# Kernel tuning notes

Hardware: AMD Instinct MI355X
Metric: run time of the kernel (lower is better)

## Reference

```python
import jax, jax.numpy as jnp
import numpy as np

N = 50000
E = 800000
IN_C, HID_C, OUT_C = 512, 256, 64
K = 10
ALPHA = 0.1


def setup_inputs() -> dict:
    key = jax.random.key(0)
    k1, k2, k3, k4, k5, k6 = jax.random.split(key, 6)
    x = jax.random.normal(k1, (N, IN_C), dtype=jnp.float32)
    edge_index = jax.random.randint(k2, (2, E), 0, N, dtype=jnp.int64)
    # Linear params (torch nn.Linear: y = x @ W.T + b), kaiming-ish scale
    W1 = jax.random.normal(k3, (HID_C, IN_C), dtype=jnp.float32) / np.sqrt(IN_C)
    b1 = jax.random.normal(k4, (HID_C,), dtype=jnp.float32) * 0.01
    W2 = jax.random.normal(k5, (OUT_C, HID_C), dtype=jnp.float32) / np.sqrt(HID_C)
    b2 = jax.random.normal(k6, (OUT_C,), dtype=jnp.float32) * 0.01
    return {"x": x, "edge_index": edge_index, "W1": W1, "b1": b1, "W2": W2, "b2": b2}


def reference(x, edge_index, W1, b1, W2, b2):
    # MLP head (dropout is identity in eval mode)
    h = jax.nn.relu(x @ W1.T + b1)          # [N, HID_C]
    z = h @ W2.T + b2                        # [N, OUT_C]

    src = edge_index[0]                      # message source
    dst = edge_index[1]                      # message target (aggregation index)

    # GCN symmetric normalization with self-loops (PyG APPNP default)
    ones = jnp.ones((E,), dtype=z.dtype)
    deg = jax.ops.segment_sum(ones, dst, num_segments=N) + 1.0  # +1 for self-loop
    dinv = jax.lax.rsqrt(deg)                # deg^{-1/2}
    edge_norm = (dinv[src] * dinv[dst])[:, None]   # [E, 1]
    self_norm = (dinv * dinv)[:, None]             # [N, 1] self-loop weight

    def step(hcur, _):
        agg = jax.ops.segment_sum(hcur[src] * edge_norm, dst, num_segments=N)
        agg = agg + hcur * self_norm
        hnew = (1.0 - ALPHA) * agg + ALPHA * z
        return hnew, None

    h_final, _ = jax.lax.scan(step, z, None, length=K)
    return h_final
```

## Files before the change

kernel.cpp:

```cpp
#include <hip/hip_runtime.h>

typedef __bf16 bf16x8 __attribute__((ext_vector_type(8)));
typedef float f32x4 __attribute__((ext_vector_type(4)));
typedef short short8 __attribute__((ext_vector_type(8)));

__device__ __forceinline__ unsigned short f2bf_u(float f) {
    unsigned u = __builtin_bit_cast(unsigned, f);
    u += 0x7FFFu + ((u >> 16) & 1u);
    return (unsigned short)(u >> 16);
}
__device__ __forceinline__ float bf2f(unsigned short h) {
    unsigned u = ((unsigned)h) << 16;
    return __builtin_bit_cast(float, u);
}
__device__ __forceinline__ float i2f(int b) { return __builtin_bit_cast(float, b); }

#define GLOAD_LDS16(gsrc, ldst)                                                        \
    __builtin_amdgcn_global_load_lds((const __attribute__((address_space(1))) void*)(gsrc), \
                                     (__attribute__((address_space(3))) void*)(ldst), 16, 0, 0)

__global__ __launch_bounds__(256)
void prep_a(const void* __restrict__ ei, const float* __restrict__ W1,
            const float* __restrict__ W2, int* __restrict__ flag,
            short* __restrict__ W1h, short* __restrict__ W1l,
            short* __restrict__ W2h, short* __restrict__ W2l) {
    const int tid = threadIdx.x;
    const int gtid = blockIdx.x * 256 + tid;
    const int gsize = gridDim.x * 256;
    if (blockIdx.x == 0) {
        unsigned v = 0;
        for (int i = tid * 2 + 1; i < 2048; i += 512) v |= ((const unsigned*)ei)[i];
        if (v) atomicOr(flag, 1);
    }
    const int n1 = 256 * 512, n2 = 64 * 256;
    for (int i = gtid; i < n1; i += gsize) {
        float w0 = W1[i];
        unsigned short h = f2bf_u(w0);
        W1h[i] = (short)h;
        W1l[i] = (short)f2bf_u(w0 - bf2f(h));
    }
    for (int i = gtid; i < n2; i += gsize) {
        float w0 = W2[i];
        unsigned short h = f2bf_u(w0);
        W2h[i] = (short)h;
        W2l[i] = (short)f2bf_u(w0 - bf2f(h));
    }
}

__global__ void convert_count_kernel(const void* __restrict__ edges, const int* __restrict__ flag,
                                     int* __restrict__ src, int* __restrict__ dst,
                                     int* __restrict__ counts, int E) {
    int e = blockIdx.x * 256 + threadIdx.x;
    if (e >= E) return;
    int s, d;
    if (*flag) { const int* p = (const int*)edges; s = p[e]; d = p[E + e]; }
    else       { const long long* p = (const long long*)edges; s = (int)p[e]; d = (int)p[E + e]; }
    src[e] = s;
    dst[e] = d;
    atomicAdd(&counts[d], 1);
}

__global__ void bsum_dinv_kernel(const int* __restrict__ counts, float* __restrict__ dinv,
                                 int* __restrict__ bs, int n) {
    __shared__ int sdata[256];
    int i = blockIdx.x * 256 + threadIdx.x;
    int v = (i < n) ? counts[i] : 0;
    if (i < n) dinv[i] = rsqrtf((float)v + 1.0f);
    sdata[threadIdx.x] = v;
    __syncthreads();
    #pragma unroll
    for (int off = 128; off > 0; off >>= 1) {
        if (threadIdx.x < off) sdata[threadIdx.x] += sdata[threadIdx.x + off];
        __syncthreads();
    }
    if (threadIdx.x == 0) bs[blockIdx.x] = sdata[0];
}

__global__ void scanbs_kernel(const int* __restrict__ bs, int* __restrict__ bsoff, int nb) {
    __shared__ int sdata[256];
    int tid = threadIdx.x;
    int v = (tid < nb) ? bs[tid] : 0;
    sdata[tid] = v;
    __syncthreads();
    #pragma unroll
    for (int off = 1; off < 256; off <<= 1) {
        int t = (tid >= off) ? sdata[tid - off] : 0;
        __syncthreads();
        sdata[tid] += t;
        __syncthreads();
    }
    if (tid < nb) bsoff[tid] = sdata[tid] - v;
}

__global__ void scanblock_kernel(const int* __restrict__ counts, const int* __restrict__ bsoff,
                                 int* __restrict__ rowptr, int* __restrict__ cursor, int n) {
    __shared__ int sdata[256];
    int tid = threadIdx.x;
    int i = blockIdx.x * 256 + tid;
    int v = (i < n) ? counts[i] : 0;
    sdata[tid] = v;
    __syncthreads();
    #pragma unroll
    for (int off = 1; off < 256; off <<= 1) {
        int t = (tid >= off) ? sdata[tid - off] : 0;
        __syncthreads();
        sdata[tid] += t;
        __syncthreads();
    }
    int excl = bsoff[blockIdx.x] + sdata[tid] - v;
    if (i < n) { rowptr[i] = excl; cursor[i] = excl; }
    if (i == n - 1) rowptr[n] = excl + v;
}

__global__ void fill_kernel(const int* __restrict__ src, const int* __restrict__ dst,
                            const float* __restrict__ dinv, int* __restrict__ cursor,
                            int2* __restrict__ csr, int E) {
    int e = blockIdx.x * 256 + threadIdx.x;
    if (e >= E) return;
    int s = src[e], d = dst[e];
    int pos = atomicAdd(&cursor[d], 1);
    float w = dinv[s] * dinv[d];
    csr[pos] = make_int2(s, __builtin_bit_cast(int, w));
}

__global__ __launch_bounds__(512)
void gemm1f_k(const float* __restrict__ x, const short* __restrict__ Bh,
              const short* __restrict__ Bl, const float* __restrict__ bias,
              short* __restrict__ C, int M) {
    extern __shared__ short lds[];
    short* sA  = lds;
    short* sBh = lds + 16384;
    short* sBl = lds + 49152;
    const int KDIM = 512, LDC = 256;
    const int tid = threadIdx.x, lane = tid & 63, wave = tid >> 6;
    const int wr = wave >> 2, wc = wave & 3;
    const int m0 = blockIdx.x * 128;
    const int lr = lane & 15, lk = lane >> 4;
    const int l8r = lane >> 3, l8u = lane & 7;
    const int tr = tid >> 3, tk = tid & 7;

    f32x4 acc[4][4];
    #pragma unroll
    for (int mi = 0; mi < 4; ++mi)
        #pragma unroll
        for (int ni = 0; ni < 4; ++ni) acc[mi][ni] = {0.f, 0.f, 0.f, 0.f};

    float4 fa[2][2];

    auto a_load = [&](int k0) {
        #pragma unroll
        for (int p = 0; p < 2; ++p) {
            int row = p * 64 + tr;
            int grow = m0 + row; if (grow > M - 1) grow = M - 1;
            const float* s = x + (size_t)grow * KDIM + k0 + tk * 8;
            fa[p][0] = *reinterpret_cast<const float4*>(s);
            fa[p][1] = *reinterpret_cast<const float4*>(s + 4);
        }
    };
    auto a_write = [&](int buf) {
        #pragma unroll
        for (int p = 0; p < 2; ++p) {
            int row = p * 64 + tr;
            short8 sh;
            sh[0] = (short)f2bf_u(fa[p][0].x); sh[1] = (short)f2bf_u(fa[p][0].y);
            sh[2] = (short)f2bf_u(fa[p][0].z); sh[3] = (short)f2bf_u(fa[p][0].w);
            sh[4] = (short)f2bf_u(fa[p][1].x); sh[5] = (short)f2bf_u(fa[p][1].y);
            sh[6] = (short)f2bf_u(fa[p][1].z); sh[7] = (short)f2bf_u(fa[p][1].w);
            *reinterpret_cast<short8*>(&sA[buf * 8192 + row * 64 + ((tk ^ (row & 7)) << 3)]) = sh;
        }
    };
    auto b_dma = [&](int buf, int k0) {
        #pragma unroll
        for (int p = 0; p < 4; ++p) {
            int row = p * 64 + wave * 8 + l8r;
            size_t goff = (size_t)row * KDIM + k0 + ((l8u ^ (row & 7)) << 3);
            GLOAD_LDS16(Bh + goff, sBh + buf * 16384 + (p * 64 + wave * 8) * 64);
            GLOAD_LDS16(Bl + goff, sBl + buf * 16384 + (p * 64 + wave * 8) * 64);
        }
    };

    a_load(0);
    b_dma(0, 0);
    asm volatile("s_waitcnt vmcnt(0)" ::: "memory");
    a_write(0);
    __syncthreads();

    int cur = 0;
    #pragma unroll 1
    for (int t = 0; t < 8; ++t) {
        const bool pf = (t < 7);
        if (pf) {
            a_load((t + 1) * 64);
            b_dma(cur ^ 1, (t + 1) * 64);
        }
        #pragma unroll
        for (int ks = 0; ks < 2; ++ks) {
            int kg = ks * 4 + lk;
            bf16x8 af[4], bhf[4], blf[4];
            #pragma unroll
            for (int mi = 0; mi < 4; ++mi) {
                int row = wr * 64 + mi * 16 + lr;
                af[mi] = *reinterpret_cast<const bf16x8*>(
                    &sA[cur * 8192 + row * 64 + ((kg ^ (row & 7)) << 3)]);
            }
            #pragma unroll
            for (int ni = 0; ni < 4; ++ni) {
                int row = wc * 64 + ni * 16 + lr;
                int idx = cur * 16384 + row * 64 + ((kg ^ (row & 7)) << 3);
                bhf[ni] = *reinterpret_cast<const bf16x8*>(&sBh[idx]);
                blf[ni] = *reinterpret_cast<const bf16x8*>(&sBl[idx]);
            }
            #pragma unroll
            for (int mi = 0; mi < 4; ++mi)
                #pragma unroll
                for (int ni = 0; ni < 4; ++ni) {
                    acc[mi][ni] = __builtin_amdgcn_mfma_f32_16x16x32_bf16(af[mi], bhf[ni], acc[mi][ni], 0, 0, 0);
                    acc[mi][ni] = __builtin_amdgcn_mfma_f32_16x16x32_bf16(af[mi], blf[ni], acc[mi][ni], 0, 0, 0);
                }
        }
        asm volatile("s_waitcnt vmcnt(0)" ::: "memory");
        if (pf) a_write(cur ^ 1);
        __syncthreads();
        cur ^= 1;
    }

    #pragma unroll
    for (int ni = 0; ni < 4; ++ni) {
        int col = wc * 64 + ni * 16 + lr;
        float bv = bias[col];
        #pragma unroll
        for (int mi = 0; mi < 4; ++mi) {
            #pragma unroll
            for (int r = 0; r < 4; ++r) {
                int row = m0 + wr * 64 + mi * 16 + lk * 4 + r;
                if (row < M) {
                    float v = fmaxf(acc[mi][ni][r] + bv, 0.0f);
                    C[(size_t)row * LDC + col] = (short)f2bf_u(v);
                }
            }
        }
    }
}

template<int KDIM, int LDC, bool AF32, bool RELU>
__device__ __forceinline__
void gemm_tile(const void* __restrict__ Av, const short* __restrict__ Bh,
               const short* __restrict__ Bl, const float* __restrict__ bias,
               short* __restrict__ C, int M, int m0, int n0,
               short* sAp, short* sBp) {
    constexpr int NT = KDIM / 64;
    const int tid  = threadIdx.x;
    const int lane = tid & 63;
    const int wave = tid >> 6;
    const int wr = wave >> 1, wc = wave & 1;
    const int lr = lane & 15;
    const int lk = lane >> 4;
    const int l8r = lane >> 3;
    const int l8u = lane & 7;
    const int tr = tid >> 3;
    const int tk = tid & 7;

    f32x4 acc[2][2];
    #pragma unroll
    for (int mi = 0; mi < 2; ++mi)
        #pragma unroll
        for (int ni = 0; ni < 2; ++ni) acc[mi][ni] = {0.f, 0.f, 0.f, 0.f};

    float4 fa[2][2];

    auto a_load = [&](int k0) {
        #pragma unroll
        for (int p = 0; p < 2; ++p) {
            int row = p * 64 + tr;
            int grow = m0 + row; if (grow > M - 1) grow = M - 1;
            const float* s = (const float*)Av + (size_t)grow * KDIM + k0 + tk * 8;
            fa[p][0] = *reinterpret_cast<const float4*>(s);
            fa[p][1] = *reinterpret_cast<const float4*>(s + 4);
        }
    };
    auto a_write = [&](int buf) {
        #pragma unroll
        for (int p = 0; p < 2; ++p) {
            int row = p * 64 + tr;
            short8 sh;
            sh[0] = (short)f2bf_u(fa[p][0].x); sh[1] = (short)f2bf_u(fa[p][0].y);
            sh[2] = (short)f2bf_u(fa[p][0].z); sh[3] = (short)f2bf_u(fa[p][0].w);
            sh[4] = (short)f2bf_u(fa[p][1].x); sh[5] = (short)f2bf_u(fa[p][1].y);
            sh[6] = (short)f2bf_u(fa[p][1].z); sh[7] = (short)f2bf_u(fa[p][1].w);
            *reinterpret_cast<short8*>(&sAp[buf * 8192 + row * 64 + ((tk ^ (row & 7)) << 3)]) = sh;
        }
    };
    auto a_dma = [&](int buf, int k0) {
        #pragma unroll
        for (int p = 0; p < 2; ++p) {
            int row = p * 64 + wave * 8 + l8r;
            int grow = m0 + row; if (grow > M - 1) grow = M - 1;
            const short* s = (const short*)Av + (size_t)grow * KDIM + k0 + ((l8u ^ (row & 7)) << 3);
            GLOAD_LDS16(s, sAp + buf * 8192 + p * 4096 + wave * 512);
        }
    };
    auto b_dma = [&](int buf, int k0) {
        int row = wave * 8 + l8r;
        size_t goff = (size_t)(n0 + row) * KDIM + k0 + ((l8u ^ (row & 7)) << 3);
        GLOAD_LDS16(Bh + goff, sBp + (buf * 2 + 0) * 4096 + wave * 512);
        GLOAD_LDS16(Bl + goff, sBp + (buf * 2 + 1) * 4096 + wave * 512);
    };

    if (AF32) {
        a_load(0);
        b_dma(0, 0);
        asm volatile("s_waitcnt vmcnt(0)" ::: "memory");
        a_write(0);
        __syncthreads();
    } else {
        a_dma(0, 0);
        b_dma(0, 0);
        asm volatile("s_waitcnt vmcnt(0)" ::: "memory");
        __builtin_amdgcn_s_barrier();
        asm volatile("" ::: "memory");
    }

    int cur = 0;
    #pragma unroll 1
    for (int t = 0; t < NT; ++t) {
        const bool pf = (t + 1 < NT);
        if (pf) {
            if (AF32) a_load((t + 1) * 64);
            else      a_dma(cur ^ 1, (t + 1) * 64);
            b_dma(cur ^ 1, (t + 1) * 64);
        }
        #pragma unroll
        for (int ks = 0; ks < 2; ++ks) {
            int kg = ks * 4 + lk;
            bf16x8 af[2], bhf[2], blf[2];
            #pragma unroll
            for (int mi = 0; mi < 2; ++mi) {
                int row = wr * 32 + mi * 16 + lr;
                af[mi] = *reinterpret_cast<const bf16x8*>(
                    &sAp[cur * 8192 + row * 64 + ((kg ^ (row & 7)) << 3)]);
            }
            #pragma unroll
            for (int ni = 0; ni < 2; ++ni) {
                int row = wc * 32 + ni * 16 + lr;
                int idx = row * 64 + ((kg ^ (row & 7)) << 3);
                bhf[ni] = *reinterpret_cast<const bf16x8*>(&sBp[(cur * 2 + 0) * 4096 + idx]);
                blf[ni] = *reinterpret_cast<const bf16x8*>(&sBp[(cur * 2 + 1) * 4096 + idx]);
            }
            #pragma unroll
            for (int mi = 0; mi < 2; ++mi)
                #pragma unroll
                for (int ni = 0; ni < 2; ++ni) {
                    acc[mi][ni] = __builtin_amdgcn_mfma_f32_16x16x32_bf16(af[mi], bhf[ni], acc[mi][ni], 0, 0, 0);
                    acc[mi][ni] = __builtin_amdgcn_mfma_f32_16x16x32_bf16(af[mi], blf[ni], acc[mi][ni], 0, 0, 0);
                }
        }
        asm volatile("s_waitcnt vmcnt(0)" ::: "memory");
        if (AF32) { if (pf) a_write(cur ^ 1); __syncthreads(); }
        else { __builtin_amdgcn_s_barrier(); asm volatile("" ::: "memory"); }
        cur ^= 1;
    }

    #pragma unroll
    for (int ni = 0; ni < 2; ++ni) {
        int col = n0 + wc * 32 + ni * 16 + lr;
        float bv = bias[col];
        #pragma unroll
        for (int mi = 0; mi < 2; ++mi) {
            #pragma unroll
            for (int r = 0; r < 4; ++r) {
                int row = m0 + wr * 32 + mi * 16 + lk * 4 + r;
                if (row < M) {
                    float v = acc[mi][ni][r] + bv;
                    if (RELU) v = fmaxf(v, 0.0f);
                    C[(size_t)row * LDC + col] = (short)f2bf_u(v);
                }
            }
        }
    }
}

__global__ __launch_bounds__(512)
void gemm1_k(const float* __restrict__ x, const short* __restrict__ W1h,
             const short* __restrict__ W1l, const float* __restrict__ b1,
             short* __restrict__ Hbf, int M) {
    __shared__ short sAp[2 * 128 * 64];
    __shared__ short sBp[2 * 2 * 64 * 64];
    int t = blockIdx.x;
    gemm_tile<512, 256, true, true>(x, W1h, W1l, b1, Hbf, M, (t >> 2) * 128, (t & 3) * 64, sAp, sBp);
}

__global__ __launch_bounds__(512)
void gemm2_k(const short* __restrict__ Hbf, const short* __restrict__ W2h,
             const short* __restrict__ W2l, const float* __restrict__ b2,
             short* __restrict__ zbf, int M) {
    __shared__ short sAp[2 * 128 * 64];
    __shared__ short sBp[2 * 2 * 64 * 64];
    gemm_tile<256, 64, false, false>(Hbf, W2h, W2l, b2, zbf, M, blockIdx.x * 128, 0, sAp, sBp);
}

__global__ __launch_bounds__(256)
void prop_step(const unsigned short* __restrict__ hin, const unsigned short* __restrict__ zbf,
               const int* __restrict__ rowptr, const int2* __restrict__ csr,
               const float* __restrict__ dinv, void* __restrict__ hout,
               int outf32, int n) {
    int node = blockIdx.x * 4 + (threadIdx.x >> 6);
    int lane = threadIdx.x & 63;
    if (node >= n) return;
    float di = dinv[node];
    int base = node << 6;
    float acc = bf2f(hin[base + lane]) * (di * di);
    int e = rowptr[node], e1 = rowptr[node + 1];

    if (e + 8 <= e1) {
        int2 r[8];
        #pragma unroll
        for (int j = 0; j < 8; ++j) r[j] = csr[e + j];
        for (; e + 16 <= e1; e += 8) {
            int2 rn[8];
            #pragma unroll
            for (int j = 0; j < 8; ++j) rn[j] = csr[e + 8 + j];
            unsigned short v[8];
            #pragma unroll
            for (int j = 0; j < 8; ++j) v[j] = hin[((unsigned)r[j].x << 6) + lane];
            #pragma unroll
            for (int j = 0; j < 8; ++j) acc = fmaf(bf2f(v[j]), i2f(r[j].y), acc);
            #pragma unroll
            for (int j = 0; j < 8; ++j) r[j] = rn[j];
        }
        {
            unsigned short v[8];
            #pragma unroll
            for (int j = 0; j < 8; ++j) v[j] = hin[((unsigned)r[j].x << 6) + lane];
            #pragma unroll
            for (int j = 0; j < 8; ++j) acc = fmaf(bf2f(v[j]), i2f(r[j].y), acc);
            e += 8;
        }
    }
    for (; e + 4 <= e1; e += 4) {
        int2 r[4]; unsigned short v[4];
        #pragma unroll
        for (int j = 0; j < 4; ++j) r[j] = csr[e + j];
        #pragma unroll
        for (int j = 0; j < 4; ++j) v[j] = hin[((unsigned)r[j].x << 6) + lane];
        #pragma unroll
        for (int j = 0; j < 4; ++j) acc = fmaf(bf2f(v[j]), i2f(r[j].y), acc);
    }
    for (; e < e1; ++e) {
        int2 r = csr[e];
        acc = fmaf(bf2f(hin[((unsigned)r.x << 6) + lane]), i2f(r.y), acc);
    }

    float res = 0.9f * acc + 0.1f * bf2f(zbf[base + lane]);
    if (outf32) ((float*)hout)[base + lane] = res;
    else        ((unsigned short*)hout)[base + lane] = f2bf_u(res);
}

extern "C" void kernel_launch(void* const* d_in, const int* in_sizes, int n_in,
                              void* d_out, int out_size, void* d_ws, size_t ws_size,
                              hipStream_t stream) {
    const float* x  = (const float*)d_in[0];
    const void*  ei = d_in[1];
    const float* W1 = (const float*)d_in[2];
    const float* b1 = (const float*)d_in[3];
    const float* W2 = (const float*)d_in[4];
    const float* b2 = (const float*)d_in[5];
    float* dout = (float*)d_out;

    const int IN_C = 512, HID_C = 256, OUT_C = 64, Ksteps = 10;
    const int N = in_sizes[0] / IN_C;
    const int E = in_sizes[1] / 2;

    char* w = (char*)d_ws;
    auto alloc = [&](size_t bytes) { char* p = w; w += (bytes + 255) & ~(size_t)255; return p; };
    int*   flag    = (int*)  alloc(4);
    int*   src32   = (int*)  alloc((size_t)E * 4);
    int*   dst32   = (int*)  alloc((size_t)E * 4);
    int*   counts  = (int*)  alloc((size_t)N * 4);
    int*   rowptr  = (int*)  alloc((size_t)(N + 1) * 4);
    int*   cursor  = (int*)  alloc((size_t)N * 4);
    float* dinv    = (float*)alloc((size_t)N * 4);
    int2*  csr     = (int2*) alloc((size_t)E * 8);
    short* W1h     = (short*)alloc((size_t)HID_C * IN_C * 2);
    short* W1l     = (short*)alloc((size_t)HID_C * IN_C * 2);
    short* W2h     = (short*)alloc((size_t)OUT_C * HID_C * 2);
    short* W2l     = (short*)alloc((size_t)OUT_C * HID_C * 2);
    short* Hbf     = (short*)alloc((size_t)N * HID_C * 2);
    unsigned short* zbf = (unsigned short*)alloc((size_t)N * OUT_C * 2);
    unsigned short* hA  = (unsigned short*)alloc((size_t)N * OUT_C * 2);
    unsigned short* hB  = (unsigned short*)alloc((size_t)N * OUT_C * 2);
    int*   bs      = (int*)  alloc(256 * 4);
    int*   bsoff   = (int*)  alloc(256 * 4);

    hipMemsetAsync(flag, 0, 4, stream);
    hipMemsetAsync(counts, 0, (size_t)N * 4, stream);

    const int egrid = (E + 255) / 256;
    const int nblk = (N + 255) / 256;
    const int mgrid = (N + 127) / 128;
    const int pgrid = (N + 3) / 4;

    prep_a<<<512, 256, 0, stream>>>(ei, W1, W2, flag, W1h, W1l, W2h, W2l);
    convert_count_kernel<<<egrid, 256, 0, stream>>>(ei, flag, src32, dst32, counts, E);
    bsum_dinv_kernel<<<nblk, 256, 0, stream>>>(counts, dinv, bs, N);
    scanbs_kernel<<<1, 256, 0, stream>>>(bs, bsoff, nblk);
    scanblock_kernel<<<nblk, 256, 0, stream>>>(counts, bsoff, rowptr, cursor, N);
    fill_kernel<<<egrid, 256, 0, stream>>>(src32, dst32, dinv, cursor, csr, E);

    constexpr int G1_LDS = 163840;
    bool big = hipFuncSetAttribute((const void*)gemm1f_k,
                                   hipFuncAttributeMaxDynamicSharedMemorySize,
                                   G1_LDS) == hipSuccess;
    if (big) {
        gemm1f_k<<<mgrid, 512, G1_LDS, stream>>>(x, W1h, W1l, b1, Hbf, N);
        if (hipGetLastError() != hipSuccess) big = false;
    }
    if (!big) {
        gemm1_k<<<mgrid * 4, 512, 0, stream>>>(x, W1h, W1l, b1, Hbf, N);
    }
    gemm2_k<<<mgrid, 512, 0, stream>>>(Hbf, W2h, W2l, b2, (short*)zbf, N);

    const unsigned short* pin = zbf;
    for (int s = 0; s < Ksteps; ++s) {
        bool last = (s == Ksteps - 1);
        void* out = last ? (void*)dout : ((s & 1) ? (void*)hB : (void*)hA);
        prop_step<<<pgrid, 256, 0, stream>>>(pin, zbf, rowptr, csr, dinv,
                                             out, last ? 1 : 0, N);
        pin = (const unsigned short*)out;
    }
}
```

Before: 452.1 us.

## Fold self-loops into CSR and split each wavefront across two edges

Each node's self-loop becomes an explicit CSR entry weighted dinv^2, so the propagation kernel no longer reads dinv or does a separate self term. The kernel now has each half-wavefront (32 lanes) handle a different edge, with every lane loading two bf16 features as a ushort2. The halves are combined with a cross-lane shuffle and only the lower half writes the output. The aim is fewer, wider gather loads and twice as many edges in flight per wave, at the cost of reading both CSR entries in every lane, a shuffle reduction, and idle upper lanes during the store.

```diff
diff --git a/kernel.cpp b/kernel.cpp
--- a/kernel.cpp
+++ b/kernel.cpp
@@ -66,7 +66,7 @@
     int i = blockIdx.x * 256 + threadIdx.x;
     int v = (i < n) ? counts[i] : 0;
     if (i < n) dinv[i] = rsqrtf((float)v + 1.0f);
-    sdata[threadIdx.x] = v;
+    sdata[threadIdx.x] = (i < n) ? (v + 1) : 0;
     __syncthreads();
     #pragma unroll
     for (int off = 128; off > 0; off >>= 1) {
@@ -93,11 +93,13 @@
 }
 
 __global__ void scanblock_kernel(const int* __restrict__ counts, const int* __restrict__ bsoff,
-                                 int* __restrict__ rowptr, int* __restrict__ cursor, int n) {
+                                 const float* __restrict__ dinv,
+                                 int* __restrict__ rowptr, int* __restrict__ cursor,
+                                 int2* __restrict__ csr, int n) {
     __shared__ int sdata[256];
     int tid = threadIdx.x;
     int i = blockIdx.x * 256 + tid;
-    int v = (i < n) ? counts[i] : 0;
+    int v = (i < n) ? (counts[i] + 1) : 0;
     sdata[tid] = v;
     __syncthreads();
     #pragma unroll
@@ -108,7 +110,12 @@
         __syncthreads();
     }
     int excl = bsoff[blockIdx.x] + sdata[tid] - v;
-    if (i < n) { rowptr[i] = excl; cursor[i] = excl; }
+    if (i < n) {
+        rowptr[i] = excl;
+        float di = dinv[i];
+        csr[excl] = make_int2(i, __builtin_bit_cast(int, di * di));
+        cursor[i] = excl + 1;
+    }
     if (i == n - 1) rowptr[n] = excl + v;
 }
 
@@ -401,58 +408,65 @@
 __global__ __launch_bounds__(256)
 void prop_step(const unsigned short* __restrict__ hin, const unsigned short* __restrict__ zbf,
                const int* __restrict__ rowptr, const int2* __restrict__ csr,
-               const float* __restrict__ dinv, void* __restrict__ hout,
-               int outf32, int n) {
+               void* __restrict__ hout, int outf32, int n) {
     int node = blockIdx.x * 4 + (threadIdx.x >> 6);
+    if (node >= n) return;
     int lane = threadIdx.x & 63;
-    if (node >= n) return;
-    float di = dinv[node];
+    int laneL = lane & 31;
+    bool hi = lane >= 32;
     int base = node << 6;
-    float acc = bf2f(hin[base + lane]) * (di * di);
     int e = rowptr[node], e1 = rowptr[node + 1];
-
-    if (e + 8 <= e1) {
-        int2 r[8];
-        #pragma unroll
-        for (int j = 0; j < 8; ++j) r[j] = csr[e + j];
-        for (; e + 16 <= e1; e += 8) {
-            int2 rn[8];
-            #pragma unroll
-            for (int j = 0; j < 8; ++j) rn[j] = csr[e + 8 + j];
-            unsigned short v[8];
-            #pragma unroll
-            for (int j = 0; j < 8; ++j) v[j] = hin[((unsigned)r[j].x << 6) + lane];
-            #pragma unroll
-            for (int j = 0; j < 8; ++j) acc = fmaf(bf2f(v[j]), i2f(r[j].y), acc);
-            #pragma unroll
-            for (int j = 0; j < 8; ++j) r[j] = rn[j];
-        }
-        {
-            unsigned short v[8];
-            #pragma unroll
-            for (int j = 0; j < 8; ++j) v[j] = hin[((unsigned)r[j].x << 6) + lane];
-            #pragma unroll
-            for (int j = 0; j < 8; ++j) acc = fmaf(bf2f(v[j]), i2f(r[j].y), acc);
-            e += 8;
-        }
-    }
-    for (; e + 4 <= e1; e += 4) {
-        int2 r[4]; unsigned short v[4];
-        #pragma unroll
-        for (int j = 0; j < 4; ++j) r[j] = csr[e + j];
-        #pragma unroll
-        for (int j = 0; j < 4; ++j) v[j] = hin[((unsigned)r[j].x << 6) + lane];
-        #pragma unroll
-        for (int j = 0; j < 4; ++j) acc = fmaf(bf2f(v[j]), i2f(r[j].y), acc);
-    }
-    for (; e < e1; ++e) {
-        int2 r = csr[e];
-        acc = fmaf(bf2f(hin[((unsigned)r.x << 6) + lane]), i2f(r.y), acc);
-    }
-
-    float res = 0.9f * acc + 0.1f * bf2f(zbf[base + lane]);
-    if (outf32) ((float*)hout)[base + lane] = res;
-    else        ((unsigned short*)hout)[base + lane] = f2bf_u(res);
+    float acc0 = 0.0f, acc1 = 0.0f;
+
+    for (; e + 16 <= e1; e += 16) {
+        int2 r[8]; ushort2 v[8];
+        #pragma unroll
+        for (int j = 0; j < 8; ++j) {
+            int2 ra = csr[e + 2 * j];
+            int2 rb = csr[e + 2 * j + 1];
+            r[j] = hi ? rb : ra;
+        }
+        #pragma unroll
+        for (int j = 0; j < 8; ++j)
+            v[j] = *reinterpret_cast<const ushort2*>(hin + (((unsigned)r[j].x) << 6) + (laneL << 1));
+        #pragma unroll
+        for (int j = 0; j < 8; ++j) {
+            float w = i2f(r[j].y);
+            acc0 = fmaf(bf2f(v[j].x), w, acc0);
+            acc1 = fmaf(bf2f(v[j].y), w, acc1);
+        }
+    }
+    for (; e + 2 <= e1; e += 2) {
+        int2 ra = csr[e];
+        int2 rb = csr[e + 1];
+        int2 rj = hi ? rb : ra;
+        ushort2 v = *reinterpret_cast<const ushort2*>(hin + (((unsigned)rj.x) << 6) + (laneL << 1));
+        float w = i2f(rj.y);
+        acc0 = fmaf(bf2f(v.x), w, acc0);
+        acc1 = fmaf(bf2f(v.y), w, acc1);
+    }
+    if (e < e1 && !hi) {
+        int2 rj = csr[e];
+        ushort2 v = *reinterpret_cast<const ushort2*>(hin + (((unsigned)rj.x) << 6) + (laneL << 1));
+        float w = i2f(rj.y);
+        acc0 = fmaf(bf2f(v.x), w, acc0);
+        acc1 = fmaf(bf2f(v.y), w, acc1);
+    }
+
+    acc0 += __shfl_xor(acc0, 32, 64);
+    acc1 += __shfl_xor(acc1, 32, 64);
+
+    if (!hi) {
+        ushort2 zz = *reinterpret_cast<const ushort2*>(zbf + base + (laneL << 1));
+        float r0 = 0.9f * acc0 + 0.1f * bf2f(zz.x);
+        float r1 = 0.9f * acc1 + 0.1f * bf2f(zz.y);
+        if (outf32) {
+            *reinterpret_cast<float2*>((float*)hout + base + (laneL << 1)) = make_float2(r0, r1);
+        } else {
+            *reinterpret_cast<ushort2*>((unsigned short*)hout + base + (laneL << 1)) =
+                make_ushort2(f2bf_u(r0), f2bf_u(r1));
+        }
+    }
 }
 
 extern "C" void kernel_launch(void* const* d_in, const int* in_sizes, int n_in,
@@ -479,7 +493,7 @@
     int*   rowptr  = (int*)  alloc((size_t)(N + 1) * 4);
     int*   cursor  = (int*)  alloc((size_t)N * 4);
     float* dinv    = (float*)alloc((size_t)N * 4);
-    int2*  csr     = (int2*) alloc((size_t)E * 8);
+    int2*  csr     = (int2*) alloc((size_t)(E + N) * 8);
     short* W1h     = (short*)alloc((size_t)HID_C * IN_C * 2);
     short* W1l     = (short*)alloc((size_t)HID_C * IN_C * 2);
     short* W2h     = (short*)alloc((size_t)OUT_C * HID_C * 2);
@@ -503,7 +517,7 @@
     convert_count_kernel<<<egrid, 256, 0, stream>>>(ei, flag, src32, dst32, counts, E);
     bsum_dinv_kernel<<<nblk, 256, 0, stream>>>(counts, dinv, bs, N);
     scanbs_kernel<<<1, 256, 0, stream>>>(bs, bsoff, nblk);
-    scanblock_kernel<<<nblk, 256, 0, stream>>>(counts, bsoff, rowptr, cursor, N);
+    scanblock_kernel<<<nblk, 256, 0, stream>>>(counts, bsoff, dinv, rowptr, cursor, csr, N);
     fill_kernel<<<egrid, 256, 0, stream>>>(src32, dst32, dinv, cursor, csr, E);
 
     constexpr int G1_LDS = 163840;
@@ -523,7 +537,7 @@
     for (int s = 0; s < Ksteps; ++s) {
         bool last = (s == Ksteps - 1);
         void* out = last ? (void*)dout : ((s & 1) ? (void*)hB : (void*)hA);
-        prop_step<<<pgrid, 256, 0, stream>>>(pin, zbf, rowptr, csr, dinv,
+        prop_step<<<pgrid, 256, 0, stream>>>(pin, zbf, rowptr, csr,
                                              out, last ? 1 : 0, N);
         pin = (const unsigned short*)out;
     }
```

Measured after the change: 502.1 us. 1.11x slower.
